# Kernel optimization log

Hardware: AMD Instinct MI355X
Metric: run time of the kernel (lower is better)

The kernel has to match this reference:

```python
import jax, jax.numpy as jnp
import numpy as np

H = 450    # hidden_size (JTNN default)
LAT = 56   # latent_size (tree_vec dim)
V = 780    # vocab size
T = 1024   # n_trees
L = 24     # nodes per tree (path topology)


def _tree_meta(Ln):
    # forward edge i: (i, i+1) eid=i ; reverse edge i: (i+1, i) eid=(Ln-1)+i
    n_f = Ln - 1
    eids, preds, srcs, dsts, labels = [], [], [], [], []
    for i in range(n_f):  # forward DFS steps
        eids.append(i); srcs.append(i); dsts.append(i + 1)
        preds.append(i - 1 if i > 0 else -1); labels.append(0)
    for k in range(n_f):  # backtrack DFS steps (reverse edges, deepest first)
        i = n_f - 1 - k
        eids.append(n_f + i); srcs.append(i + 1); dsts.append(i)
        preds.append(n_f + i + 1 if i < n_f - 1 else -1); labels.append(1)
    # incoming edges of the dst node v (for the node 'pull' h = sum of m)
    in1 = [d - 1 if d > 0 else -1 for d in dsts]
    in2 = [n_f + d if d < n_f else -1 for d in dsts]
    meta = [np.asarray(a, np.int32) for a in (eids, preds, srcs, dsts, in1, in2)]
    return meta, np.asarray(labels, np.float32)


def setup_inputs():
    key = jax.random.key(0)
    ks = jax.random.split(key, 12)
    s = 0.05
    return {
        "wid": jax.random.randint(ks[0], (T, L), 0, V, dtype=jnp.int32),
        "tree_vec": jax.random.normal(ks[1], (T, LAT), jnp.float32),
        "emb": jax.random.normal(ks[2], (V, H)) * s,
        "W_w": jax.random.normal(ks[3], (H + LAT, H)) * s, "W_b": jnp.zeros((H,)),
        "U_w": jax.random.normal(ks[4], (2 * H + LAT, H)) * s, "U_b": jnp.zeros((H,)),
        "Wo_w": jax.random.normal(ks[5], (H, V)) * s, "Wo_b": jnp.zeros((V,)),
        "Us_w": jax.random.normal(ks[6], (H, 1)) * s, "Us_b": jnp.zeros((1,)),
        "Wz_w": jax.random.normal(ks[7], (2 * H, H)) * s, "Wz_b": jnp.zeros((H,)),
        "Wr_w": jax.random.normal(ks[8], (H, H)) * s,
        "Ur_w": jax.random.normal(ks[9], (H, H)) * s, "Ur_b": jnp.zeros((H,)),
        "Wh_w": jax.random.normal(ks[10], (2 * H, H)) * s, "Wh_b": jnp.zeros((H,)),
    }


def reference(wid, tree_vec, emb, W_w, W_b, U_w, U_b, Wo_w, Wo_b, Us_w, Us_b,
              Wz_w, Wz_b, Wr_w, Ur_w, Ur_b, Wh_w, Wh_b):
    Tn, Ln = wid.shape
    n_f = Ln - 1
    nE = 2 * n_f
    meta, labels = _tree_meta(Ln)
    xs = tuple(jnp.asarray(a) for a in meta)
    x = emb[wid]                                  # [T, L, H] node features
    m0 = jnp.zeros((Tn, nE, H), x.dtype)
    rm0 = jnp.zeros((Tn, nE, H), x.dtype)

    def step(carry, sx_):
        m, rm = carry
        eid, pred, src, dst, i1, i2 = sx_
        gp = jnp.maximum(pred, 0)
        s = jnp.where(pred >= 0, m[:, gp], 0.0)        # line-graph pull: sum of m
        arm = jnp.where(pred >= 0, rm[:, gp], 0.0)     # accum_rm
        sxn = x[:, src]                                # src_x
        dxn = x[:, dst]                                # dst_x
        z = jax.nn.sigmoid(jnp.concatenate([sxn, s], 1) @ Wz_w + Wz_b)
        mt = jnp.tanh(jnp.concatenate([sxn, arm], 1) @ Wh_w + Wh_b)
        m_new = (1.0 - z) * s + z * mt
        r = jax.nn.sigmoid(dxn @ Wr_w + m_new @ Ur_w + Ur_b)
        m = m.at[:, eid].set(m_new)
        rm = rm.at[:, eid].set(r * m_new)
        # node pull on v: h_v = sum of m over incoming edges (post edge update)
        h_v = (jnp.where(i1 >= 0, m[:, jnp.maximum(i1, 0)], 0.0)
               + jnp.where(i2 >= 0, m[:, jnp.maximum(i2, 0)], 0.0))
        return (m, rm), (h_v, dxn)

    (_, _), (hs, xvs) = jax.lax.scan(step, (m0, rm0), xs)  # [nE, T, H] each

    tv_steps = jnp.broadcast_to(tree_vec, (nE, Tn, LAT))
    p_in = jnp.concatenate([
        jnp.concatenate([x[:, 0], jnp.zeros((Tn, H), x.dtype), tree_vec], 1),
        jnp.concatenate([xvs, hs, tv_steps], -1).reshape(-1, 2 * H + LAT),
    ], 0)
    q_in = jnp.concatenate([
        jnp.concatenate([jnp.zeros((Tn, H), x.dtype), tree_vec], 1),
        jnp.concatenate([hs[:n_f], tv_steps[:n_f]], -1).reshape(-1, H + LAT),
    ], 0)
    p_targets = jnp.concatenate([jnp.repeat(jnp.asarray(1.0 - labels), Tn),
                                 jnp.zeros((Tn,), jnp.float32)])
    q_targets = wid.T.reshape(-1)

    q_logits = jax.nn.relu(q_in @ W_w + W_b) @ Wo_w + Wo_b
    p_logit = (jax.nn.relu(p_in @ U_w + U_b) @ Us_w + Us_b)[:, 0]
    p_loss = jnp.sum(p_targets * jax.nn.softplus(-p_logit)
                     + (1.0 - p_targets) * jax.nn.softplus(p_logit)) / Tn
    logp = jax.nn.log_softmax(q_logits, -1)
    q_loss = -jnp.sum(jnp.take_along_axis(logp, q_targets[:, None], 1)) / Tn
    p_acc = jnp.mean(((p_logit > 0).astype(jnp.int32) == p_targets.astype(jnp.int32)).astype(jnp.float32))
    q_acc = jnp.mean((jnp.argmax(q_logits, 1) == q_targets).astype(jnp.float32))
    return (q_loss, p_loss, q_acc, p_acc)
```

## Files before the change

### kernel.cpp

```cpp
#include <hip/hip_runtime.h>
#include <hip/hip_bf16.h>
#include <math.h>

#define H 450
#define HP 464
#define KP 480
#define LAT 56
#define V 780
#define LW 24
#define NE 46
#define NF 23
#define SLOT (1024*HP)
#define SROWS 2048
#define QROWS (24*1024)
#define PROWS (47*1024)
#define PTGT  (23*1024)
#define QBLK 6144
#define XBSZ ((size_t)QROWS * H)

typedef __hip_bfloat16 bf16;
typedef __attribute__((ext_vector_type(8))) short short8;
typedef __attribute__((ext_vector_type(4))) float f32x4;

#define MFMA16(a,b,c) __builtin_amdgcn_mfma_f32_16x16x32_bf16(a,b,c,0,0,0)

__device__ __forceinline__ float sigm(float x) { return 1.f / (1.f + expf(-x)); }
__device__ __forceinline__ float toF(bf16 x) { return __bfloat162float(x); }
__device__ __forceinline__ void stV(float* p, float v) { *p = v; }
__device__ __forceinline__ void stV(bf16* p, float v) { *p = __float2bfloat16(v); }
__device__ __forceinline__ short8 ld8(const bf16* p) { return *reinterpret_cast<const short8*>(p); }

__device__ __forceinline__ void gl_lds(const bf16* g, bf16* l) {
    __builtin_amdgcn_global_load_lds(
        (const __attribute__((address_space(1))) void*)g,
        (__attribute__((address_space(3))) void*)l, 16, 0, 0);
}

__device__ __forceinline__ void xcd_decode(int b, int C, int& row0, int& col0) {
    int rres = b & 7;
    int colt = (b >> 3) % C;
    int g    = b / (8 * C);
    row0 = (rres + 8 * g) * 64;
    col0 = colt * 64;
}
__device__ __forceinline__ void xcd_decode128(int b, int C, int& row0, int& col0) {
    int rres = b & 7;
    int colt = (b >> 3) % C;
    int g    = b / (8 * C);
    row0 = (rres + 8 * g) * 128;
    col0 = colt * 128;
}

__global__ __launch_bounds__(256)
void make_bt(const float* __restrict__ src, int K, int N, int ld,
             bf16* __restrict__ dst, int npad) {
    int idx = blockIdx.x * 256 + threadIdx.x;
    if (idx >= npad * KP) return;
    int n = idx / KP, k = idx - n * KP;
    float v = (n < N && k < K) ? src[(size_t)k * ld + n] : 0.f;
    dst[idx] = __float2bfloat16(v);
}

__global__ __launch_bounds__(256)
void pack_bias(const float* __restrict__ zb, const float* __restrict__ hb,
               const float* __restrict__ rb, float* __restrict__ bias4) {
    int i = blockIdx.x * 256 + threadIdx.x;
    if (i >= 1856) return;
    float v = 0.f;
    if (i < 450)       v = zb[i];
    else if (i < 900)  v = hb[i - 450];
    else if (i < 1350) v = rb[i - 900];
    bias4[i] = v;
}

__global__ __launch_bounds__(256)
void zero_init(float* __restrict__ out, float* __restrict__ Sb, int n) {
    int i = blockIdx.x * 256 + threadIdx.x;
    if (i < 4) out[i] = 0.f;
    if (i < n) Sb[i] = 0.f;
}

__global__ __launch_bounds__(256)
void gather_x(const float* __restrict__ emb, const int* __restrict__ wid,
              bf16* __restrict__ x_all) {
    int e = blockIdx.x * 256 + threadIdx.x;
    if (e >= 24 * 1024 * 225) return;
    int row = e / 225, h2 = e - row * 225;
    int t = row >> 10, n = row & 1023;
    int v = wid[n * LW + t];
    float2 x = ((const float2*)(emb + (size_t)v * H))[h2];
    bf16* dst = x_all + (size_t)row * HP + 2 * h2;
    dst[0] = __float2bfloat16(x.x);
    dst[1] = __float2bfloat16(x.y);
}

template<typename TC>
__global__ __launch_bounds__(256)
void gemm128(const bf16* __restrict__ A, int lda,
             const bf16* __restrict__ Bt, int N, int cblk,
             TC* __restrict__ C, int ldc,
             const float* __restrict__ bias,
             const float* __restrict__ addrow, int addld, int relu) {
    __shared__ bf16 As[128 * 32];
    __shared__ bf16 Bs[128 * 32];
    int tid = threadIdx.x;
    int lane = tid & 63, wave = tid >> 6;
    int wx = wave & 1, wy = wave >> 1;
    int lrow = lane & 15, quad = lane >> 4;
    int perm = ((quad + (lrow >> 1)) & 3) * 8;
    int row0, col0;
    xcd_decode128(blockIdx.x, cblk, row0, col0);
    f32x4 acc[4][4] = {};
    for (int k0i = 0; k0i < 15; k0i++) {
        int k0 = k0i * 32;
#pragma unroll
        for (int r = 0; r < 2; r++) {
            int tt = r * 256 + tid;
            int row = tt >> 2, cl = tt & 3;
            int cg = (cl - (row >> 1)) & 3;
            gl_lds(A  + (size_t)(row0 + row) * lda + k0 + cg * 8, As + tt * 8);
            gl_lds(Bt + (size_t)(col0 + row) * KP  + k0 + cg * 8, Bs + tt * 8);
        }
        __syncthreads();
        short8 a[4], b[4];
#pragma unroll
        for (int f = 0; f < 4; f++)
            a[f] = ld8(As + (wy * 64 + f * 16 + lrow) * 32 + perm);
#pragma unroll
        for (int f = 0; f < 4; f++)
            b[f] = ld8(Bs + (wx * 64 + f * 16 + lrow) * 32 + perm);
#pragma unroll
        for (int fi = 0; fi < 4; fi++)
#pragma unroll
            for (int fj = 0; fj < 4; fj++)
                acc[fi][fj] = MFMA16(a[fi], b[fj], acc[fi][fj]);
        __syncthreads();
    }
#pragma unroll
    for (int fi = 0; fi < 4; fi++)
#pragma unroll
        for (int e = 0; e < 4; e++) {
            int r = row0 + wy * 64 + fi * 16 + quad * 4 + e;
#pragma unroll
            for (int fj = 0; fj < 4; fj++) {
                int c = col0 + wx * 64 + fj * 16 + lrow;
                if (c >= N) continue;
                float v = acc[fi][fj][e];
                if (bias) v += bias[c];
                if (addrow) v += addrow[(size_t)(r & 1023) * addld + c];
                if (relu) v = fmaxf(v, 0.f);
                stV(&C[(size_t)r * ldc + c], v);
            }
        }
}

__global__ __launch_bounds__(256)
void gemm128_pre(const bf16* __restrict__ A,
                 const bf16* __restrict__ Bt,
                 bf16* __restrict__ X0,
                 const float* __restrict__ bias4) {
    __shared__ bf16 As[128 * 32];
    __shared__ bf16 Bs[128 * 32];
    int tid = threadIdx.x;
    int lane = tid & 63, wave = tid >> 6;
    int wx = wave & 1, wy = wave >> 1;
    int lrow = lane & 15, quad = lane >> 4;
    int perm = ((quad + (lrow >> 1)) & 3) * 8;
    int row0, col0;
    xcd_decode128(blockIdx.x, 15, row0, col0);
    f32x4 acc[4][4] = {};
    for (int k0i = 0; k0i < 15; k0i++) {
        int k0 = k0i * 32;
#pragma unroll
        for (int r = 0; r < 2; r++) {
            int tt = r * 256 + tid;
            int row = tt >> 2, cl = tt & 3;
            int cg = (cl - (row >> 1)) & 3;
            gl_lds(A  + (size_t)(row0 + row) * HP + k0 + cg * 8, As + tt * 8);
            gl_lds(Bt + (size_t)(col0 + row) * KP + k0 + cg * 8, Bs + tt * 8);
        }
        __syncthreads();
        short8 a[4], b[4];
#pragma unroll
        for (int f = 0; f < 4; f++)
            a[f] = ld8(As + (wy * 64 + f * 16 + lrow) * 32 + perm);
#pragma unroll
        for (int f = 0; f < 4; f++)
            b[f] = ld8(Bs + (wx * 64 + f * 16 + lrow) * 32 + perm);
#pragma unroll
        for (int fi = 0; fi < 4; fi++)
#pragma unroll
            for (int fj = 0; fj < 4; fj++)
                acc[fi][fj] = MFMA16(a[fi], b[fj], acc[fi][fj]);
        __syncthreads();
    }
#pragma unroll
    for (int fi = 0; fi < 4; fi++)
#pragma unroll
        for (int e = 0; e < 4; e++) {
            int r = row0 + wy * 64 + fi * 16 + quad * 4 + e;
#pragma unroll
            for (int fj = 0; fj < 4; fj++) {
                int c = col0 + wx * 64 + fj * 16 + lrow;
                if (c >= 1800) continue;
                int mm = c / 450;
                int cc = c - mm * 450;
                float v = acc[fi][fj][e] + bias4[c];
                X0[(size_t)mm * XBSZ + (size_t)r * H + cc] = __float2bfloat16(v);
            }
        }
}

__global__ __launch_bounds__(256)
void p_gemm128(const bf16* __restrict__ hs, const bf16* __restrict__ UbT,
               const bf16* __restrict__ XUa, const float* __restrict__ Ptv,
               const float* __restrict__ Us, float* __restrict__ pl) {
    __shared__ bf16 As[128 * 32];
    __shared__ bf16 Bs[128 * 32];
    int tid = threadIdx.x;
    int lane = tid & 63, wave = tid >> 6;
    int wx = wave & 1, wy = wave >> 1;
    int lrow = lane & 15, quad = lane >> 4;
    int perm = ((quad + (lrow >> 1)) & 3) * 8;
    int row0, col0;
    xcd_decode128(blockIdx.x, 4, row0, col0);
    f32x4 acc[4][4] = {};
    for (int k0i = 0; k0i < 15; k0i++) {
        int k0 = k0i * 32;
#pragma unroll
        for (int r = 0; r < 2; r++) {
            int tt = r * 256 + tid;
            int row = tt >> 2, cl = tt & 3;
            int cg = (cl - (row >> 1)) & 3;
            gl_lds(hs  + (size_t)(row0 + row) * HP + k0 + cg * 8, As + tt * 8);
            gl_lds(UbT + (size_t)(col0 + row) * KP + k0 + cg * 8, Bs + tt * 8);
        }
        __syncthreads();
        short8 a[4], b[4];
#pragma unroll
        for (int f = 0; f < 4; f++)
            a[f] = ld8(As + (wy * 64 + f * 16 + lrow) * 32 + perm);
#pragma unroll
        for (int f = 0; f < 4; f++)
            b[f] = ld8(Bs + (wx * 64 + f * 16 + lrow) * 32 + perm);
#pragma unroll
        for (int fi = 0; fi < 4; fi++)
#pragma unroll
            for (int fj = 0; fj < 4; fj++)
                acc[fi][fj] = MFMA16(a[fi], b[fj], acc[fi][fj]);
        __syncthreads();
    }
#pragma unroll
    for (int fi = 0; fi < 4; fi++)
#pragma unroll
        for (int e = 0; e < 4; e++) {
            int r = row0 + wy * 64 + fi * 16 + quad * 4 + e;
            int t = r >> 10, n = r & 1023;
            int dst = (t < 23) ? (t + 1) : (45 - t);
            float part = 0.f;
#pragma unroll
            for (int fj = 0; fj < 4; fj++) {
                int c = col0 + wx * 64 + fj * 16 + lrow;
                if (c < H) {
                    float h = fmaxf(acc[fi][fj][e] + toF(XUa[((size_t)dst * 1024 + n) * H + c])
                                    + Ptv[(size_t)n * H + c], 0.f);
                    part += h * Us[c];
                }
            }
#pragma unroll
            for (int off = 1; off < 16; off <<= 1)
                part += __shfl_xor(part, off);
            if (lrow == 0) atomicAdd(&pl[1024 + r], part);
        }
}

__global__ __launch_bounds__(256)
void tv_gemm(const float* __restrict__ tv, const float* __restrict__ Wlat,
             const float* __restrict__ bias, float* __restrict__ out) {
    int n = blockIdx.y;
    int c = blockIdx.x * 256 + threadIdx.x;
    __shared__ float tvs[LAT];
    if (threadIdx.x < LAT) tvs[threadIdx.x] = tv[n * LAT + threadIdx.x];
    __syncthreads();
    if (c < H) {
        float a = bias[c];
#pragma unroll 8
        for (int k = 0; k < LAT; k++) a += tvs[k] * Wlat[(size_t)k * H + c];
        out[(size_t)n * H + c] = a;
    }
}

__global__ __launch_bounds__(256)
void scan_k1(const bf16* __restrict__ AsF, const bf16* __restrict__ AsB,
             const bf16* __restrict__ Arm,
             const bf16* __restrict__ BzT, const bf16* __restrict__ BhT,
             const bf16* __restrict__ Xz, const bf16* __restrict__ Xh,
             float* __restrict__ Sb, bf16* __restrict__ hsF, bf16* __restrict__ hsB,
             int u, int skip) {
    int tid = threadIdx.x;
    int lane = tid & 63, wave = tid >> 6;
    int wx = wave & 1, wy = wave >> 1;
    int lrow = lane & 15, quad = lane >> 4;
    int row0, col0;
    xcd_decode(blockIdx.x, 8, row0, col0);
    bool fwd = row0 < 1024;
    int rb = row0 & 1023;
    f32x4 az[2][2] = {}, ah[2][2] = {};
    if (!skip) {
        const bf16* As = (fwd ? AsF : AsB) + (size_t)(rb + wy * 32 + lrow) * HP + quad * 8;
        const bf16* Ar = Arm + (size_t)(row0 + wy * 32 + lrow) * HP + quad * 8;
        const bf16* bz0 = BzT + (size_t)(col0 + wx * 32 + lrow) * KP + quad * 8;
        const bf16* bh0 = BhT + (size_t)(col0 + wx * 32 + lrow) * KP + quad * 8;
        for (int k = 0; k < 15; k++) {
            short8 s0 = ld8(As + k * 32);
            short8 s1 = ld8(As + (size_t)16 * HP + k * 32);
            short8 r0 = ld8(Ar + k * 32);
            short8 r1 = ld8(Ar + (size_t)16 * HP + k * 32);
            short8 z0 = ld8(bz0 + k * 32);
            short8 z1 = ld8(bz0 + 16 * KP + k * 32);
            short8 h0 = ld8(bh0 + k * 32);
            short8 h1 = ld8(bh0 + 16 * KP + k * 32);
            az[0][0] = MFMA16(s0, z0, az[0][0]);
            az[0][1] = MFMA16(s0, z1, az[0][1]);
            az[1][0] = MFMA16(s1, z0, az[1][0]);
            az[1][1] = MFMA16(s1, z1, az[1][1]);
            ah[0][0] = MFMA16(r0, h0, ah[0][0]);
            ah[0][1] = MFMA16(r0, h1, ah[0][1]);
            ah[1][0] = MFMA16(r1, h0, ah[1][0]);
            ah[1][1] = MFMA16(r1, h1, ah[1][1]);
        }
    }
    int src = fwd ? u : 23 - u;
    bf16* hso = fwd ? hsF : hsB;
#pragma unroll
    for (int i = 0; i < 2; i++)
#pragma unroll
        for (int e = 0; e < 4; e++) {
            int r = row0 + wy * 32 + i * 16 + quad * 4 + e;
            int n = r & 1023;
#pragma unroll
            for (int j = 0; j < 2; j++) {
                int c = col0 + wx * 32 + j * 16 + lrow;
                if (c >= H) continue;
                float zp = az[i][j][e] + toF(Xz[((size_t)src * 1024 + n) * H + c]);
                float hp = ah[i][j][e] + toF(Xh[((size_t)src * 1024 + n) * H + c]);
                float s  = Sb[(size_t)r * H + c];
                float z  = sigm(zp);
                float mt = tanhf(hp);
                float mn = (1.f - z) * s + z * mt;
                Sb[(size_t)r * H + c] = mn;
                hso[(size_t)n * HP + c] = __float2bfloat16(mn);
            }
        }
}

__global__ __launch_bounds__(256)
void scan_k2(const bf16* __restrict__ AmF, const bf16* __restrict__ AmB,
             const bf16* __restrict__ UrT, const bf16* __restrict__ Xr,
             const float* __restrict__ Sb, bf16* __restrict__ RMb, int u) {
    int tid = threadIdx.x;
    int lane = tid & 63, wave = tid >> 6;
    int wx = wave & 1, wy = wave >> 1;
    int lrow = lane & 15, quad = lane >> 4;
    int row0, col0;
    xcd_decode(blockIdx.x, 8, row0, col0);
    bool fwd = row0 < 1024;
    int rb = row0 & 1023;
    const bf16* Am = (fwd ? AmF : AmB) + (size_t)(rb + wy * 32 + lrow) * HP + quad * 8;
    const bf16* b0 = UrT + (size_t)(col0 + wx * 32 + lrow) * KP + quad * 8;
    f32x4 acc[2][2] = {};
    for (int k = 0; k < 15; k++) {
        short8 a0 = ld8(Am + k * 32);
        short8 a1 = ld8(Am + (size_t)16 * HP + k * 32);
        short8 w0 = ld8(b0 + k * 32);
        short8 w1 = ld8(b0 + 16 * KP + k * 32);
        acc[0][0] = MFMA16(a0, w0, acc[0][0]);
        acc[0][1] = MFMA16(a0, w1, acc[0][1]);
        acc[1][0] = MFMA16(a1, w0, acc[1][0]);
        acc[1][1] = MFMA16(a1, w1, acc[1][1]);
    }
    int dst = fwd ? (u + 1) : (22 - u);
#pragma unroll
    for (int i = 0; i < 2; i++)
#pragma unroll
        for (int e = 0; e < 4; e++) {
            int r = row0 + wy * 32 + i * 16 + quad * 4 + e;
            int n = r & 1023;
#pragma unroll
            for (int j = 0; j < 2; j++) {
                int c = col0 + wx * 32 + j * 16 + lrow;
                if (c >= H) continue;
                float rp = acc[i][j][e] + toF(Xr[((size_t)dst * 1024 + n) * H + c]);
                float rr = sigm(rp);
                RMb[(size_t)r * HP + c] = __float2bfloat16(rr * Sb[(size_t)r * H + c]);
            }
        }
}

__global__ __launch_bounds__(256)
void hv_fixup(bf16* __restrict__ hs) {
    int idx = blockIdx.x * 256 + threadIdx.x;
    if (idx >= 22 * SLOT) return;
    int tl = idx / SLOT;
    int rem = idx - tl * SLOT;
    size_t a = (size_t)(23 + tl) * SLOT + rem;
    size_t b = (size_t)(21 - tl) * SLOT + rem;
    hs[a] = __float2bfloat16(toF(hs[a]) + toF(hs[b]));
}

__global__ __launch_bounds__(256)
void q_root(const float* __restrict__ Qtv, bf16* __restrict__ qh) {
    int idx = blockIdx.x * 256 + threadIdx.x;
    if (idx >= 1024 * H) return;
    int n = idx / H, c = idx - n * H;
    qh[(size_t)n * HP + c] = __float2bfloat16(fmaxf(Qtv[idx], 0.f));
}

__global__ __launch_bounds__(256)
void q_reduce(const float* __restrict__ ql, const int* __restrict__ wid,
              float* __restrict__ qred) {
    int wave = threadIdx.x >> 6, lane = threadIdx.x & 63;
    int r = blockIdx.x * 4 + wave;
    int t = r >> 10, n = r & 1023;
    int tgt = wid[n * LW + t];
    const float4* row4 = (const float4*)(ql + (size_t)r * V);
    float m = -3.4e38f, s = 0.f; int mi = 0x7fffffff;
#pragma unroll
    for (int k = 0; k < 4; k++) {
        int c4 = lane + 64 * k;
        if (c4 < 195) {
            float4 v4 = row4[c4];
            float vv[4] = {v4.x, v4.y, v4.z, v4.w};
#pragma unroll
            for (int e = 0; e < 4; e++) {
                float v = vv[e];
                if (v > m) { s = s * __expf(m - v) + 1.f; m = v; mi = c4 * 4 + e; }
                else s += __expf(v - m);
            }
        }
    }
#pragma unroll
    for (int off = 1; off < 64; off <<= 1) {
        float m2 = __shfl_xor(m, off);
        float s2 = __shfl_xor(s, off);
        int   i2 = __shfl_xor(mi, off);
        if (m2 > m || (m2 == m && i2 < mi)) {
            s = s2 + s * __expf(m - m2);
            m = m2; mi = i2;
        } else {
            s = s + s2 * __expf(m2 - m);
        }
    }
    __shared__ float lred[4][2];
    if (lane == 0) {
        float lse = m + logf(s);
        lred[wave][0] = lse - ql[(size_t)r * V + tgt];
        lred[wave][1] = (mi == tgt) ? 1.f : 0.f;
    }
    __syncthreads();
    if (threadIdx.x == 0) {
        qred[blockIdx.x * 2]     = lred[0][0] + lred[1][0] + lred[2][0] + lred[3][0];
        qred[blockIdx.x * 2 + 1] = lred[0][1] + lred[1][1] + lred[2][1] + lred[3][1];
    }
}

__global__ __launch_bounds__(256)
void q_final(const float* __restrict__ qred, float* __restrict__ out) {
    int tid = threadIdx.x;
    float L = 0.f, A = 0.f;
    for (int i = tid; i < QBLK; i += 256) { L += qred[2 * i]; A += qred[2 * i + 1]; }
    __shared__ float s1[256], s2[256];
    s1[tid] = L; s2[tid] = A;
    __syncthreads();
    for (int k = 128; k > 0; k >>= 1) {
        if (tid < k) { s1[tid] += s1[tid + k]; s2[tid] += s2[tid + k]; }
        __syncthreads();
    }
    if (tid == 0) {
        out[0] = s1[0] * (1.f / 1024.f);
        out[2] = s2[0] * (1.f / 24576.f);
    }
}

__global__ __launch_bounds__(256)
void p_init(float* __restrict__ pl, const float* __restrict__ Us_b) {
    int idx = blockIdx.x * 256 + threadIdx.x;
    if (idx < PROWS) pl[idx] = Us_b[0];
}

__global__ __launch_bounds__(256)
void p_root(const bf16* __restrict__ XUa, const float* __restrict__ Ptv,
            const float* __restrict__ Us, float* __restrict__ pl) {
    int n = blockIdx.x;
    int tid = threadIdx.x;
    const bf16* xa = XUa + (size_t)n * H;
    const float* pt = Ptv + (size_t)n * H;
    float s = 0.f;
    for (int c = tid; c < H; c += 256)
        s += fmaxf(toF(xa[c]) + pt[c], 0.f) * Us[c];
    __shared__ float red[256];
    red[tid] = s;
    __syncthreads();
    for (int k = 128; k > 0; k >>= 1) {
        if (tid < k) red[tid] += red[tid + k];
        __syncthreads();
    }
    if (tid == 0) atomicAdd(&pl[n], red[0]);
}

__global__ __launch_bounds__(256)
void p_final(const float* __restrict__ pl, float* __restrict__ out) {
    int r = blockIdx.x * 256 + threadIdx.x;
    int tid = threadIdx.x;
    float loss = 0.f, acc = 0.f;
    if (r < PROWS) {
        float l = pl[r];
        int tgt = (r < PTGT) ? 1 : 0;
        float x = tgt ? -l : l;
        loss = fmaxf(x, 0.f) + log1pf(expf(-fabsf(x)));
        int pred = (l > 0.f) ? 1 : 0;
        acc = (pred == tgt) ? 1.f : 0.f;
    }
    __shared__ float s1[256], s2[256];
    s1[tid] = loss; s2[tid] = acc;
    __syncthreads();
    for (int k = 128; k > 0; k >>= 1) {
        if (tid < k) { s1[tid] += s1[tid + k]; s2[tid] += s2[tid + k]; }
        __syncthreads();
    }
    if (tid == 0) {
        atomicAdd(&out[1], s1[0] * (1.f / 1024.f));
        atomicAdd(&out[3], s2[0] * (1.f / 48128.f));
    }
}

extern "C" void kernel_launch(void* const* d_in, const int* in_sizes, int n_in,
                              void* d_out, int out_size, void* d_ws, size_t ws_size,
                              hipStream_t stream) {
    const int*   wid  = (const int*)  d_in[0];
    const float* tv   = (const float*)d_in[1];
    const float* emb  = (const float*)d_in[2];
    const float* W_w  = (const float*)d_in[3];
    const float* W_b  = (const float*)d_in[4];
    const float* U_w  = (const float*)d_in[5];
    const float* U_b  = (const float*)d_in[6];
    const float* Wo_w = (const float*)d_in[7];
    const float* Wo_b = (const float*)d_in[8];
    const float* Us_w = (const float*)d_in[9];
    const float* Us_b = (const float*)d_in[10];
    const float* Wz_w = (const float*)d_in[11];
    const float* Wz_b = (const float*)d_in[12];
    const float* Wr_w = (const float*)d_in[13];
    const float* Ur_w = (const float*)d_in[14];
    const float* Ur_b = (const float*)d_in[15];
    const float* Wh_w = (const float*)d_in[16];
    const float* Wh_b = (const float*)d_in[17];
    float* out = (float*)d_out;

    char* base = (char*)d_ws;
    const size_t XBb = XBSZ * 2;
    bf16*  Xz   = (bf16*)(base);
    bf16*  Xh   = (bf16*)(base + XBb);
    bf16*  Xr   = (bf16*)(base + 2 * XBb);
    bf16*  XUa  = (bf16*)(base + 3 * XBb);
    bf16*  hs   = (bf16*)(base + 4 * XBb);
    bf16*  x_all = hs;
    char*  p1   = base + 4 * XBb + (size_t)NE * SLOT * 2;
    bf16*  RMb  = (bf16*)p1;                p1 += (size_t)SROWS * HP * 2;
    float* Sb   = (float*)p1;               p1 += (size_t)SROWS * H * 4;
    float* Qtv  = (float*)p1;               p1 += (size_t)1024 * H * 4;
    float* Ptv  = (float*)p1;               p1 += (size_t)1024 * H * 4;
    float* pl   = (float*)p1;               p1 += (size_t)PROWS * 4;
    float* qred = (float*)p1;               p1 += (size_t)QBLK * 2 * 4;
    float* bias4 = (float*)p1;              p1 += (size_t)1856 * 4;
    bf16*  BT   = (bf16*)p1;
    bf16* BT4   = BT;
    bf16* WzbT  = BT + (size_t)1856 * KP;
    bf16* WhbT  = WzbT + (size_t)512 * KP;
    bf16* UrT   = WhbT + (size_t)512 * KP;
    bf16* UbT   = UrT  + (size_t)512 * KP;
    bf16* WtopT = UbT  + (size_t)512 * KP;
    bf16* WoT   = WtopT + (size_t)512 * KP;
    bf16*  qh = (bf16*)base;
    float* ql = (float*)(base + (size_t)QROWS * HP * 2);

    zero_init<<<(SROWS * H + 255) / 256, 256, 0, stream>>>(out, Sb, SROWS * H);
    int btg = (512 * KP + 255) / 256;
    int btg450 = (450 * KP + 255) / 256;
    make_bt<<<btg450, 256, 0, stream>>>(Wz_w, H, H, H, BT4,                        450);
    make_bt<<<btg450, 256, 0, stream>>>(Wh_w, H, H, H, BT4 + (size_t)450 * KP,     450);
    make_bt<<<btg450, 256, 0, stream>>>(Wr_w, H, H, H, BT4 + (size_t)900 * KP,     450);
    make_bt<<<(506 * KP + 255) / 256, 256, 0, stream>>>(U_w, H, H, H, BT4 + (size_t)1350 * KP, 506);
    pack_bias<<<8, 256, 0, stream>>>(Wz_b, Wh_b, Ur_b, bias4);
    make_bt<<<btg, 256, 0, stream>>>(Wz_w + 450*450,  H, H, H, WzbT, 512);
    make_bt<<<btg, 256, 0, stream>>>(Wh_w + 450*450,  H, H, H, WhbT, 512);
    make_bt<<<btg, 256, 0, stream>>>(Ur_w,            H, H, H, UrT,  512);
    make_bt<<<btg, 256, 0, stream>>>(U_w + 450*450,   H, H, H, UbT,  512);
    make_bt<<<btg, 256, 0, stream>>>(W_w,             H, H, H, WtopT, 512);
    make_bt<<<(896 * KP + 255) / 256, 256, 0, stream>>>(Wo_w, H, V, V, WoT, 896);

    gather_x<<<(24 * 1024 * 225 + 255) / 256, 256, 0, stream>>>(emb, wid, x_all);
    gemm128_pre<<<(QROWS / 128) * 15, 256, 0, stream>>>(x_all, BT4, Xz, bias4);

    tv_gemm<<<dim3(2, 1024), 256, 0, stream>>>(tv, W_w + 450*450, W_b, Qtv);
    tv_gemm<<<dim3(2, 1024), 256, 0, stream>>>(tv, U_w + 900*450, U_b, Ptv);

    for (int u = 0; u < 23; u++) {
        const bf16* AsF = hs + (size_t)(u - 1) * SLOT;
        const bf16* AsB = hs + (size_t)(22 + u) * SLOT;
        scan_k1<<<256, 256, 0, stream>>>(AsF, AsB, RMb, WzbT, WhbT, Xz, Xh,
                                         Sb, hs + (size_t)u * SLOT,
                                         hs + (size_t)(23 + u) * SLOT, u, u == 0 ? 1 : 0);
        if (u < 22)
            scan_k2<<<256, 256, 0, stream>>>(hs + (size_t)u * SLOT, hs + (size_t)(23 + u) * SLOT,
                                             UrT, Xr, Sb, RMb, u);
    }
    hv_fixup<<<(22 * SLOT + 255) / 256, 256, 0, stream>>>(hs);

    p_init<<<(PROWS + 255) / 256, 256, 0, stream>>>(pl, Us_b);
    p_root<<<1024, 256, 0, stream>>>(XUa, Ptv, Us_w, pl);
    p_gemm128<<<(PROWS - 1024) / 128 * 4, 256, 0, stream>>>(hs, UbT, XUa, Ptv, Us_w, pl);
    p_final<<<PROWS / 256, 256, 0, stream>>>(pl, out);

    q_root<<<(1024 * H + 255) / 256, 256, 0, stream>>>(Qtv, qh);
    gemm128<bf16><<<(NF * 1024 / 128) * 4, 256, 0, stream>>>(hs, HP, WtopT, H, 4,
                                                             qh + (size_t)1024 * HP, HP,
                                                             (const float*)nullptr, Qtv, H, 1);
    gemm128<float><<<(QROWS / 128) * 7, 256, 0, stream>>>(qh, HP, WoT, V, 7, ql, V,
                                                          Wo_b, (const float*)nullptr, H, 0);
    q_reduce<<<QBLK, 256, 0, stream>>>(ql, wid, qred);
    q_final<<<1, 256, 0, stream>>>(qred, out);

    (void)in_sizes; (void)n_in; (void)out_size; (void)ws_size;
}
```

Baseline: 1.104 ms.

## Fuse per-step scan kernels into one persistent cooperative kernel with grid barriers

Replaces the 45 separate scan_k1/scan_k2 launches of the sequential message-passing scan with one cooperative persistent kernel. Each of the 256 blocks loops over all steps and synchronises the grid with a software atomic barrier after each phase. This removes per-launch overhead and inter-kernel gaps. In exchange it depends on all 256 blocks being co-resident, and each barrier costs device-scope fences and spinning.

```diff
diff --git a/kernel.cpp b/kernel.cpp
--- a/kernel.cpp
+++ b/kernel.cpp
@@ -51,6 +51,24 @@
     col0 = colt * 128;
 }
 
+__device__ __forceinline__ void gbar(int* bar, int nblk, int id, int tid) {
+    __threadfence();
+    __syncthreads();
+    if (tid == 0) {
+        if (__hip_atomic_fetch_add(&bar[0], 1, __ATOMIC_ACQ_REL,
+                                   __HIP_MEMORY_SCOPE_AGENT) == nblk - 1) {
+            __hip_atomic_store(&bar[0], 0, __ATOMIC_RELAXED, __HIP_MEMORY_SCOPE_AGENT);
+            __hip_atomic_store(&bar[1], id, __ATOMIC_RELEASE, __HIP_MEMORY_SCOPE_AGENT);
+        } else {
+            while (__hip_atomic_load(&bar[1], __ATOMIC_ACQUIRE,
+                                     __HIP_MEMORY_SCOPE_AGENT) < id)
+                __builtin_amdgcn_s_sleep(1);
+        }
+    }
+    __syncthreads();
+    __threadfence();
+}
+
 __global__ __launch_bounds__(256)
 void make_bt(const float* __restrict__ src, int K, int N, int ld,
              bf16* __restrict__ dst, int npad) {
@@ -74,9 +92,11 @@
 }
 
 __global__ __launch_bounds__(256)
-void zero_init(float* __restrict__ out, float* __restrict__ Sb, int n) {
+void zero_init(float* __restrict__ out, float* __restrict__ Sb, int n,
+               int* __restrict__ bar) {
     int i = blockIdx.x * 256 + threadIdx.x;
     if (i < 4) out[i] = 0.f;
+    if (i < 2) bar[i] = 0;
     if (i < n) Sb[i] = 0.f;
 }
 
@@ -291,12 +311,12 @@
 }
 
 __global__ __launch_bounds__(256)
-void scan_k1(const bf16* __restrict__ AsF, const bf16* __restrict__ AsB,
-             const bf16* __restrict__ Arm,
-             const bf16* __restrict__ BzT, const bf16* __restrict__ BhT,
-             const bf16* __restrict__ Xz, const bf16* __restrict__ Xh,
-             float* __restrict__ Sb, bf16* __restrict__ hsF, bf16* __restrict__ hsB,
-             int u, int skip) {
+void scan_persist(bf16* __restrict__ hs, bf16* __restrict__ RMb,
+                  const bf16* __restrict__ WzbT, const bf16* __restrict__ WhbT,
+                  const bf16* __restrict__ UrT,
+                  const bf16* __restrict__ Xz, const bf16* __restrict__ Xh,
+                  const bf16* __restrict__ Xr, float* __restrict__ Sb,
+                  int* __restrict__ bar) {
     int tid = threadIdx.x;
     int lane = tid & 63, wave = tid >> 6;
     int wx = wave & 1, wy = wave >> 1;
@@ -305,96 +325,97 @@
     xcd_decode(blockIdx.x, 8, row0, col0);
     bool fwd = row0 < 1024;
     int rb = row0 & 1023;
-    f32x4 az[2][2] = {}, ah[2][2] = {};
-    if (!skip) {
-        const bf16* As = (fwd ? AsF : AsB) + (size_t)(rb + wy * 32 + lrow) * HP + quad * 8;
-        const bf16* Ar = Arm + (size_t)(row0 + wy * 32 + lrow) * HP + quad * 8;
-        const bf16* bz0 = BzT + (size_t)(col0 + wx * 32 + lrow) * KP + quad * 8;
-        const bf16* bh0 = BhT + (size_t)(col0 + wx * 32 + lrow) * KP + quad * 8;
-        for (int k = 0; k < 15; k++) {
-            short8 s0 = ld8(As + k * 32);
-            short8 s1 = ld8(As + (size_t)16 * HP + k * 32);
-            short8 r0 = ld8(Ar + k * 32);
-            short8 r1 = ld8(Ar + (size_t)16 * HP + k * 32);
-            short8 z0 = ld8(bz0 + k * 32);
-            short8 z1 = ld8(bz0 + 16 * KP + k * 32);
-            short8 h0 = ld8(bh0 + k * 32);
-            short8 h1 = ld8(bh0 + 16 * KP + k * 32);
-            az[0][0] = MFMA16(s0, z0, az[0][0]);
-            az[0][1] = MFMA16(s0, z1, az[0][1]);
-            az[1][0] = MFMA16(s1, z0, az[1][0]);
-            az[1][1] = MFMA16(s1, z1, az[1][1]);
-            ah[0][0] = MFMA16(r0, h0, ah[0][0]);
-            ah[0][1] = MFMA16(r0, h1, ah[0][1]);
-            ah[1][0] = MFMA16(r1, h0, ah[1][0]);
-            ah[1][1] = MFMA16(r1, h1, ah[1][1]);
-        }
-    }
-    int src = fwd ? u : 23 - u;
-    bf16* hso = fwd ? hsF : hsB;
-#pragma unroll
-    for (int i = 0; i < 2; i++)
-#pragma unroll
-        for (int e = 0; e < 4; e++) {
-            int r = row0 + wy * 32 + i * 16 + quad * 4 + e;
-            int n = r & 1023;
-#pragma unroll
-            for (int j = 0; j < 2; j++) {
-                int c = col0 + wx * 32 + j * 16 + lrow;
-                if (c >= H) continue;
-                float zp = az[i][j][e] + toF(Xz[((size_t)src * 1024 + n) * H + c]);
-                float hp = ah[i][j][e] + toF(Xh[((size_t)src * 1024 + n) * H + c]);
-                float s  = Sb[(size_t)r * H + c];
-                float z  = sigm(zp);
-                float mt = tanhf(hp);
-                float mn = (1.f - z) * s + z * mt;
-                Sb[(size_t)r * H + c] = mn;
-                hso[(size_t)n * HP + c] = __float2bfloat16(mn);
+    int barid = 0;
+
+    for (int u = 0; u < 23; u++) {
+        {
+            f32x4 az[2][2] = {}, ah[2][2] = {};
+            if (u > 0) {
+                const bf16* As = hs + (size_t)(fwd ? (u - 1) : (22 + u)) * SLOT
+                                 + (size_t)(rb + wy * 32 + lrow) * HP + quad * 8;
+                const bf16* Ar = RMb + (size_t)(row0 + wy * 32 + lrow) * HP + quad * 8;
+                const bf16* bz0 = WzbT + (size_t)(col0 + wx * 32 + lrow) * KP + quad * 8;
+                const bf16* bh0 = WhbT + (size_t)(col0 + wx * 32 + lrow) * KP + quad * 8;
+                for (int k = 0; k < 15; k++) {
+                    short8 s0 = ld8(As + k * 32);
+                    short8 s1 = ld8(As + (size_t)16 * HP + k * 32);
+                    short8 r0 = ld8(Ar + k * 32);
+                    short8 r1 = ld8(Ar + (size_t)16 * HP + k * 32);
+                    short8 z0 = ld8(bz0 + k * 32);
+                    short8 z1 = ld8(bz0 + 16 * KP + k * 32);
+                    short8 h0 = ld8(bh0 + k * 32);
+                    short8 h1 = ld8(bh0 + 16 * KP + k * 32);
+                    az[0][0] = MFMA16(s0, z0, az[0][0]);
+                    az[0][1] = MFMA16(s0, z1, az[0][1]);
+                    az[1][0] = MFMA16(s1, z0, az[1][0]);
+                    az[1][1] = MFMA16(s1, z1, az[1][1]);
+                    ah[0][0] = MFMA16(r0, h0, ah[0][0]);
+                    ah[0][1] = MFMA16(r0, h1, ah[0][1]);
+                    ah[1][0] = MFMA16(r1, h0, ah[1][0]);
+                    ah[1][1] = MFMA16(r1, h1, ah[1][1]);
+                }
             }
-        }
-}
-
-__global__ __launch_bounds__(256)
-void scan_k2(const bf16* __restrict__ AmF, const bf16* __restrict__ AmB,
-             const bf16* __restrict__ UrT, const bf16* __restrict__ Xr,
-             const float* __restrict__ Sb, bf16* __restrict__ RMb, int u) {
-    int tid = threadIdx.x;
-    int lane = tid & 63, wave = tid >> 6;
-    int wx = wave & 1, wy = wave >> 1;
-    int lrow = lane & 15, quad = lane >> 4;
-    int row0, col0;
-    xcd_decode(blockIdx.x, 8, row0, col0);
-    bool fwd = row0 < 1024;
-    int rb = row0 & 1023;
-    const bf16* Am = (fwd ? AmF : AmB) + (size_t)(rb + wy * 32 + lrow) * HP + quad * 8;
-    const bf16* b0 = UrT + (size_t)(col0 + wx * 32 + lrow) * KP + quad * 8;
-    f32x4 acc[2][2] = {};
-    for (int k = 0; k < 15; k++) {
-        short8 a0 = ld8(Am + k * 32);
-        short8 a1 = ld8(Am + (size_t)16 * HP + k * 32);
-        short8 w0 = ld8(b0 + k * 32);
-        short8 w1 = ld8(b0 + 16 * KP + k * 32);
-        acc[0][0] = MFMA16(a0, w0, acc[0][0]);
-        acc[0][1] = MFMA16(a0, w1, acc[0][1]);
-        acc[1][0] = MFMA16(a1, w0, acc[1][0]);
-        acc[1][1] = MFMA16(a1, w1, acc[1][1]);
-    }
-    int dst = fwd ? (u + 1) : (22 - u);
-#pragma unroll
-    for (int i = 0; i < 2; i++)
-#pragma unroll
-        for (int e = 0; e < 4; e++) {
-            int r = row0 + wy * 32 + i * 16 + quad * 4 + e;
-            int n = r & 1023;
-#pragma unroll
-            for (int j = 0; j < 2; j++) {
-                int c = col0 + wx * 32 + j * 16 + lrow;
-                if (c >= H) continue;
-                float rp = acc[i][j][e] + toF(Xr[((size_t)dst * 1024 + n) * H + c]);
-                float rr = sigm(rp);
-                RMb[(size_t)r * HP + c] = __float2bfloat16(rr * Sb[(size_t)r * H + c]);
+            int src = fwd ? u : 23 - u;
+            bf16* hso = hs + (size_t)(fwd ? u : 23 + u) * SLOT;
+#pragma unroll
+            for (int i = 0; i < 2; i++)
+#pragma unroll
+                for (int e = 0; e < 4; e++) {
+                    int r = row0 + wy * 32 + i * 16 + quad * 4 + e;
+                    int n = r & 1023;
+#pragma unroll
+                    for (int j = 0; j < 2; j++) {
+                        int c = col0 + wx * 32 + j * 16 + lrow;
+                        if (c >= H) continue;
+                        float zp = az[i][j][e] + toF(Xz[((size_t)src * 1024 + n) * H + c]);
+                        float hp = ah[i][j][e] + toF(Xh[((size_t)src * 1024 + n) * H + c]);
+                        float s  = Sb[(size_t)r * H + c];
+                        float z  = sigm(zp);
+                        float mt = tanhf(hp);
+                        float mn = (1.f - z) * s + z * mt;
+                        Sb[(size_t)r * H + c] = mn;
+                        hso[(size_t)n * HP + c] = __float2bfloat16(mn);
+                    }
+                }
+        }
+        barid++;
+        gbar(bar, 256, barid, tid);
+
+        if (u < 22) {
+            const bf16* Am = hs + (size_t)(fwd ? u : 23 + u) * SLOT
+                             + (size_t)(rb + wy * 32 + lrow) * HP + quad * 8;
+            const bf16* b0 = UrT + (size_t)(col0 + wx * 32 + lrow) * KP + quad * 8;
+            f32x4 acc[2][2] = {};
+            for (int k = 0; k < 15; k++) {
+                short8 a0 = ld8(Am + k * 32);
+                short8 a1 = ld8(Am + (size_t)16 * HP + k * 32);
+                short8 w0 = ld8(b0 + k * 32);
+                short8 w1 = ld8(b0 + 16 * KP + k * 32);
+                acc[0][0] = MFMA16(a0, w0, acc[0][0]);
+                acc[0][1] = MFMA16(a0, w1, acc[0][1]);
+                acc[1][0] = MFMA16(a1, w0, acc[1][0]);
+                acc[1][1] = MFMA16(a1, w1, acc[1][1]);
             }
-        }
+            int dst = fwd ? (u + 1) : (22 - u);
+#pragma unroll
+            for (int i = 0; i < 2; i++)
+#pragma unroll
+                for (int e = 0; e < 4; e++) {
+                    int r = row0 + wy * 32 + i * 16 + quad * 4 + e;
+                    int n = r & 1023;
+#pragma unroll
+                    for (int j = 0; j < 2; j++) {
+                        int c = col0 + wx * 32 + j * 16 + lrow;
+                        if (c >= H) continue;
+                        float rp = acc[i][j][e] + toF(Xr[((size_t)dst * 1024 + n) * H + c]);
+                        float rr = sigm(rp);
+                        RMb[(size_t)r * HP + c] = __float2bfloat16(rr * Sb[(size_t)r * H + c]);
+                    }
+                }
+            barid++;
+            gbar(bar, 256, barid, tid);
+        }
+    }
 }
 
 __global__ __launch_bounds__(256)
@@ -572,6 +593,7 @@
     float* Ptv  = (float*)p1;               p1 += (size_t)1024 * H * 4;
     float* pl   = (float*)p1;               p1 += (size_t)PROWS * 4;
     float* qred = (float*)p1;               p1 += (size_t)QBLK * 2 * 4;
+    int*   bar  = (int*)p1;                 p1 += 16;
     float* bias4 = (float*)p1;              p1 += (size_t)1856 * 4;
     bf16*  BT   = (bf16*)p1;
     bf16* BT4   = BT;
@@ -584,7 +606,7 @@
     bf16*  qh = (bf16*)base;
     float* ql = (float*)(base + (size_t)QROWS * HP * 2);
 
-    zero_init<<<(SROWS * H + 255) / 256, 256, 0, stream>>>(out, Sb, SROWS * H);
+    zero_init<<<(SROWS * H + 255) / 256, 256, 0, stream>>>(out, Sb, SROWS * H, bar);
     int btg = (512 * KP + 255) / 256;
     int btg450 = (450 * KP + 255) / 256;
     make_bt<<<btg450, 256, 0, stream>>>(Wz_w, H, H, H, BT4,                        450);
@@ -605,15 +627,12 @@
     tv_gemm<<<dim3(2, 1024), 256, 0, stream>>>(tv, W_w + 450*450, W_b, Qtv);
     tv_gemm<<<dim3(2, 1024), 256, 0, stream>>>(tv, U_w + 900*450, U_b, Ptv);
 
-    for (int u = 0; u < 23; u++) {
-        const bf16* AsF = hs + (size_t)(u - 1) * SLOT;
-        const bf16* AsB = hs + (size_t)(22 + u) * SLOT;
-        scan_k1<<<256, 256, 0, stream>>>(AsF, AsB, RMb, WzbT, WhbT, Xz, Xh,
-                                         Sb, hs + (size_t)u * SLOT,
-                                         hs + (size_t)(23 + u) * SLOT, u, u == 0 ? 1 : 0);
-        if (u < 22)
-            scan_k2<<<256, 256, 0, stream>>>(hs + (size_t)u * SLOT, hs + (size_t)(23 + u) * SLOT,
-                                             UrT, Xr, Sb, RMb, u);
+    {
+        void* sargs[] = { (void*)&hs, (void*)&RMb, (void*)&WzbT, (void*)&WhbT,
+                          (void*)&UrT, (void*)&Xz, (void*)&Xh, (void*)&Xr,
+                          (void*)&Sb, (void*)&bar };
+        hipLaunchCooperativeKernel(reinterpret_cast<void*>(scan_persist),
+                                   dim3(256), dim3(256), sargs, 0, stream);
     }
     hv_fixup<<<(22 * SLOT + 255) / 256, 256, 0, stream>>>(hs);
 
```

Result: slower. 4.193 ms (+279.9%).
